# Kernel tuning notes

Measured on AMD Instinct MI355X. Metric: run time of the kernel, lower is better.

## Reference

```python
import jax, jax.numpy as jnp
import numpy as np

N, D, L = 1000, 256, 7  # nodes, feature dim, layers (hardcoded in the torch module)
B = 64


def setup_inputs() -> dict:
    key = jax.random.key(0)
    ks = jax.random.split(key, 8)
    x = jax.random.normal(ks[0], (B, N, D), dtype=jnp.float32)
    # binary adjacency mask (diagonal is forced to 1 inside reference, as in torch)
    adj = (jax.random.uniform(ks[1], (B, N, N)) < 0.05).astype(jnp.float32)
    # stacked per-layer weights; torch Linear convention: y = x @ W.T + b
    W_attn = jax.random.normal(ks[2], (L, D, D), dtype=jnp.float32) * 0.01
    b_attn = jnp.zeros((L, D), jnp.float32)
    W0 = jax.random.normal(ks[3], (L, D, D), dtype=jnp.float32) * 0.05
    b0 = jnp.zeros((L, D), jnp.float32)
    W1 = jax.random.normal(ks[4], (L, D, D), dtype=jnp.float32) * 0.05
    b1 = jnp.zeros((L, D), jnp.float32)
    Wf = jax.random.normal(ks[5], (D, D), dtype=jnp.float32) * 0.05
    bf = jnp.zeros((D,), jnp.float32)
    return {"x": x, "adj": adj, "W_attn": W_attn, "b_attn": b_attn,
            "W0": W0, "b0": b0, "W1": W1, "b1": b1, "Wf": Wf, "bf": bf}


def reference(x, adj, W_attn, b_attn, W0, b0, W1, b1, Wf, bf):
    idx = jnp.arange(N)
    adj = adj.at[:, idx, idx].set(1.0)              # self-loops forced on
    eps_eye = (1e-5 * jnp.eye(N, dtype=x.dtype))    # added before masking
    for l in range(L):
        x0 = x
        q = x @ W_attn[l].T + b_attn[l]             # [B,N,D]
        s = jax.nn.sigmoid(jnp.einsum('bid,bjd->bij', q, x))  # [B,N,N]
        s = (s + eps_eye) * adj                     # mask by adjacency
        s = s / jnp.sum(s, axis=-1, keepdims=True)  # row-sum normalize
        x = jnp.einsum('bij,bjd->bid', s, x)        # weighted aggregate
        x = jax.nn.relu(x @ W0[l].T + b0[l])
        x = jax.nn.relu(x @ W1[l].T + b1[l])
        x = x + x0                                  # residual
    return x @ Wf.T + bf
```

## Files before the change

### kernel.cpp

```cpp
#include <hip/hip_runtime.h>
#include <hip/hip_bf16.h>

#define B_ 64
#define N_ 1000
#define NP 1024
#define D_ 256
#define L_ 7
#define MP (B_*NP)
#define PKB 262144

typedef unsigned short u16;
typedef __attribute__((ext_vector_type(4))) float f32x4;
typedef __bf16 bf16x8 __attribute__((ext_vector_type(8)));

static __device__ __forceinline__ u16 f2bf(float f) {
  __hip_bfloat16 h = __float2bfloat16(f);
  return *reinterpret_cast<u16*>(&h);
}
static __device__ __forceinline__ float bf2f(u16 u) {
  __hip_bfloat16 h;
  *reinterpret_cast<u16*>(&h) = u;
  return __bfloat162float(h);
}

static __device__ __forceinline__ void gl_lds16(const u16* g, u16* l) {
  __builtin_amdgcn_global_load_lds(
      (const __attribute__((address_space(1))) void*)g,
      (__attribute__((address_space(3))) void*)l, 16, 0, 0);
}

__global__ __launch_bounds__(64) void pack_mask_k(const float* __restrict__ adj,
                                                  unsigned long long* __restrict__ mask) {
  int row = blockIdx.x;
  int b = row / N_, i = row - b * N_;
  int lane = threadIdx.x;
  const float* arow = adj + (size_t)(b * N_ + i) * N_;
  #pragma unroll
  for (int j0 = 0; j0 < NP; j0 += 64) {
    int j = j0 + lane;
    bool on = (j < N_) && (arow[j] != 0.0f || j == i);
    unsigned long long m = __ballot(on);
    if (lane == 0) mask[((size_t)(b * NP + i)) * 16 + (j0 >> 6)] = m;
  }
}

__global__ __launch_bounds__(256) void conv_w_k(const float* __restrict__ Wa,
                                                const float* __restrict__ W0,
                                                const float* __restrict__ W1,
                                                const float* __restrict__ Wf,
                                                u16* __restrict__ wpk) {
  int T = blockIdx.x * 256 + threadIdx.x;
  const int NW = 3 * L_ + 1;
  if (T >= NW * 128 * 64) return;
  int lane = T & 63;
  int fid = T >> 6;
  int k = fid & 7, f = (fid >> 3) & 3, by = (fid >> 5) & 3, w = fid >> 7;
  const float* src;
  if (w < L_) src = Wa + (size_t)w * D_ * D_;
  else if (w < 2 * L_) src = W0 + (size_t)(w - L_) * D_ * D_;
  else if (w < 3 * L_) src = W1 + (size_t)(w - 2 * L_) * D_ * D_;
  else src = Wf;
  int row = by * 64 + f * 16 + (lane & 15);
  int col = k * 32 + ((lane >> 4) << 3);
  const float* s = src + (size_t)row * D_ + col;
  u16 out8[8];
  #pragma unroll
  for (int e = 0; e < 8; e++) out8[e] = f2bf(s[e]);
  *reinterpret_cast<bf16x8*>(wpk + (size_t)T * 8) =
      *reinterpret_cast<bf16x8*>(out8);
}

__global__ __launch_bounds__(256) void prep_x_k(const float* __restrict__ x,
                                                float* __restrict__ xc,
                                                u16* __restrict__ xb) {
  size_t t = (size_t)blockIdx.x * blockDim.x + threadIdx.x;
  const size_t total = (size_t)B_ * N_ * D_;
  if (t < total) {
    int b = (int)(t / (N_ * D_));
    int rem = (int)(t - (size_t)b * (N_ * D_));
    size_t o = (size_t)b * NP * D_ + rem;
    float v = x[t];
    xc[o] = v;
    xb[o] = f2bf(v);
  }
  const size_t padTotal = (size_t)B_ * (NP - N_) * D_;
  if (t < padTotal) {
    int b = (int)(t / ((NP - N_) * D_));
    int rem = (int)(t - (size_t)b * ((NP - N_) * D_));
    size_t o = (size_t)b * NP * D_ + (size_t)N_ * D_ + rem;
    xc[o] = 0.f;
    xb[o] = 0;
  }
}

__global__ __launch_bounds__(256) void pack_both_k(const u16* __restrict__ xb,
                                                   u16* __restrict__ xpk,
                                                   u16* __restrict__ pvpk) {
  __shared__ u16 t[64][65];
  int b = blockIdx.z;
  int cc = blockIdx.x;
  int bd = blockIdx.y;
  int i0 = cc * 64, d0 = bd * 64;
  int tid = threadIdx.x;
  int tx = tid & 63, ty = tid >> 6;
  const u16* src = xb + (size_t)b * NP * D_;
  #pragma unroll
  for (int r = ty; r < 64; r += 4)
    t[r][tx] = src[(size_t)(i0 + r) * D_ + d0 + tx];
  __syncthreads();
  int lane = tid & 63, q = tid >> 6;
  int l4 = lane >> 4, l15 = lane & 15;
  int dh = bd >> 1, dcb = (bd & 1) * 4;
  u16* dstp = pvpk + (size_t)b * PKB;
  #pragma unroll
  for (int kk = 0; kk < 2; kk++) {
    int frag = cc * 32 + dh * 16 + (dcb + q) * 2 + kk;
    bf16x8 v;
    #pragma unroll
    for (int e = 0; e < 8; e++)
      v[e] = *reinterpret_cast<const __bf16*>(&t[kk * 32 + (l4 << 3) + e][q * 16 + l15]);
    *reinterpret_cast<bf16x8*>(dstp + (size_t)frag * 512 + lane * 8) = v;
  }
  u16* dstq = xpk + (size_t)b * PKB;
  #pragma unroll
  for (int kk = 0; kk < 2; kk++) {
    int frag = cc * 32 + q * 8 + (2 * bd + kk);
    bf16x8 v;
    #pragma unroll
    for (int e = 0; e < 8; e++)
      v[e] = *reinterpret_cast<const __bf16*>(&t[l15 + 16 * q][kk * 32 + (l4 << 3) + e]);
    *reinterpret_cast<bf16x8*>(dstq + (size_t)frag * 512 + lane * 8) = v;
  }
}

template <int MODE, int APK>
__global__ __launch_bounds__(256) void linear_k(const u16* __restrict__ A,
                                                const u16* __restrict__ W,
                                                const float* __restrict__ bias,
                                                u16* __restrict__ outb,
                                                float* __restrict__ xc,
                                                u16* __restrict__ xbp,
                                                float* __restrict__ outf) {
  int lane = threadIdx.x & 63;
  int wv = threadIdx.x >> 6;
  int rbase = blockIdx.x * 64 + wv * 16;
  int cbase = blockIdx.y * 64;
  f32x4 acc[4] = {};
  const u16* Ar;
  if (APK) Ar = A + ((size_t)(rbase >> 4) << 12) + lane * 8;
  else     Ar = A + (size_t)(rbase + (lane & 15)) * D_ + ((lane >> 4) << 3);
  const u16* Wr = W + (size_t)blockIdx.y * (32 * 512) + lane * 8;
  #pragma unroll
  for (int k = 0; k < 8; k++) {
    bf16x8 a = APK ? *reinterpret_cast<const bf16x8*>(Ar + k * 512)
                   : *reinterpret_cast<const bf16x8*>(Ar + k * 32);
    #pragma unroll
    for (int f = 0; f < 4; f++) {
      bf16x8 bb = *reinterpret_cast<const bf16x8*>(Wr + (f * 8 + k) * 512);
      acc[f] = __builtin_amdgcn_mfma_f32_16x16x32_bf16(a, bb, acc[f], 0, 0, 0);
    }
  }
  int r0 = rbase + ((lane >> 4) << 2);
  int col = cbase + (lane & 15);
  #pragma unroll
  for (int f = 0; f < 4; f++) {
    int c = col + f * 16;
    float bv = bias[c];
    #pragma unroll
    for (int r = 0; r < 4; r++) {
      int row = r0 + r;
      float v = acc[f][r] + bv;
      if (MODE == 3) {
        int b = row >> 10, i = row & (NP - 1);
        if (i < N_) outf[((size_t)b * N_ + i) * D_ + c] = v;
      } else {
        size_t dst = ((size_t)(row >> 4) << 12) + ((c >> 5) << 9) +
                     ((((c >> 3) & 3) * 16 + (row & 15)) << 3) + (c & 7);
        outb[dst] = f2bf(v);
      }
    }
  }
}

__global__ __launch_bounds__(256) void mlp_fused_k(const u16* __restrict__ A,
                                                   const u16* __restrict__ W0p,
                                                   const float* __restrict__ bias0,
                                                   const u16* __restrict__ W1p,
                                                   const float* __restrict__ bias1,
                                                   u16* __restrict__ xpk,
                                                   float* __restrict__ xc,
                                                   u16* __restrict__ pvpk) {
  __shared__ u16 h0lds[8192];
  int blk = blockIdx.x;
  int lane = threadIdx.x & 63;
  int wv = threadIdx.x >> 6;
  int rsub = wv & 1, ch = wv >> 1;
  int l15 = lane & 15, l4 = lane >> 4;

  const u16* Ar = A + (size_t)(blk * 32 + rsub * 16 + l15) * D_ + (l4 << 3);
  const u16* w0b = W0p + (size_t)(ch * 64) * 512 + lane * 8;
  #pragma unroll
  for (int hf = 0; hf < 2; hf++) {
    f32x4 acc1[4] = {};
    __builtin_amdgcn_s_setprio(1);
    #pragma unroll
    for (int k = 0; k < 8; k++) {
      bf16x8 a = *reinterpret_cast<const bf16x8*>(Ar + k * 32);
      #pragma unroll
      for (int ff = 0; ff < 4; ff++) {
        bf16x8 bb = *reinterpret_cast<const bf16x8*>(
            w0b + (hf * 32 + ff * 8 + k) * 512);
        acc1[ff] = __builtin_amdgcn_mfma_f32_16x16x32_bf16(a, bb, acc1[ff], 0, 0, 0);
      }
    }
    __builtin_amdgcn_s_setprio(0);
    #pragma unroll
    for (int ff = 0; ff < 4; ff++) {
      int fc = hf * 4 + ff;
      int c = ch * 128 + fc * 16 + l15;
      float bv = bias0[c];
      int base = rsub * 4096 + (ch * 4 + (fc >> 1)) * 512 +
                 (((fc * 2 + (l15 >> 3)) & 3) * 16 + l4 * 4) * 8 + (l15 & 7);
      #pragma unroll
      for (int r = 0; r < 4; r++)
        h0lds[base + r * 8] = f2bf(fmaxf(acc1[ff][r] + bv, 0.f));
    }
  }
  __syncthreads();

  const u16* w1b = W1p + (size_t)(ch * 64) * 512 + lane * 8;
  int r0g = blk * 32 + rsub * 16 + l4 * 4;
  #pragma unroll
  for (int hf = 0; hf < 2; hf++) {
    f32x4 acc2[4] = {};
    __builtin_amdgcn_s_setprio(1);
    #pragma unroll
    for (int k = 0; k < 8; k++) {
      bf16x8 a = *reinterpret_cast<const bf16x8*>(&h0lds[rsub * 4096 + k * 512 + lane * 8]);
      #pragma unroll
      for (int ff = 0; ff < 4; ff++) {
        bf16x8 bb = *reinterpret_cast<const bf16x8*>(
            w1b + (hf * 32 + ff * 8 + k) * 512);
        acc2[ff] = __builtin_amdgcn_mfma_f32_16x16x32_bf16(a, bb, acc2[ff], 0, 0, 0);
      }
    }
    __builtin_amdgcn_s_setprio(0);
    #pragma unroll
    for (int ff = 0; ff < 4; ff++) {
      int fc = hf * 4 + ff;
      int c = ch * 128 + fc * 16 + l15;
      float bv = bias1[c];
      #pragma unroll
      for (int r = 0; r < 4; r++) {
        int row = r0g + r;
        float v = fmaxf(acc2[ff][r] + bv, 0.f);
        size_t o = (size_t)row * D_ + c;
        float nv = v + xc[o];
        xc[o] = nv;
        u16 q16 = f2bf(nv);
        size_t dx = ((size_t)(row >> 4) << 12) + ((c >> 5) << 9) +
                    ((((c >> 3) & 3) * 16 + (row & 15)) << 3) + (c & 7);
        xpk[dx] = q16;
        int bb2 = row >> 10, ri = row & (NP - 1);
        size_t fragp = (size_t)(ri >> 6) * 32 + (c >> 7) * 16 +
                       (((c >> 4) & 7) * 2) + ((ri >> 5) & 1);
        size_t dp = (size_t)bb2 * PKB + fragp * 512 +
                    ((((ri >> 3) & 3) * 16 + (c & 15)) << 3) + (ri & 7);
        pvpk[dp] = q16;
      }
    }
  }
}

__global__ __launch_bounds__(512) void attn_fused_k(const u16* __restrict__ qpk,
                                                    const u16* __restrict__ xpk,
                                                    const u16* __restrict__ pvpk,
                                                    const unsigned long long* __restrict__ mask,
                                                    u16* __restrict__ yb) {
  __shared__ u16 xlds[16384];
  __shared__ u16 plds[2][64][72];
  __shared__ float dlds[8][16];
  int wg = blockIdx.x;
  int xcd = wg & 7, slot = wg >> 3;
  int b = xcd * 8 + (slot >> 4);
  int rb = slot & 15;
  int rbase = rb * 64;
  int lane = threadIdx.x & 63;
  int wv = threadIdx.x >> 6;
  int rsub = wv & 3, jh = wv >> 2;
  int l15 = lane & 15, l4 = lane >> 4;
  int rowL = rsub * 16 + l4 * 4;

  const u16* qpkB = qpk + ((((size_t)b * NP + rbase + rsub * 16) >> 4) << 12) + lane * 8;
  const u16* xpkC = xpk + (size_t)b * PKB;
  const u16* pvkB = pvpk + (size_t)b * PKB + (size_t)((wv >> 2) * 16 + (wv & 3) * 4) * 512 + lane * 8;
  const unsigned long long* mB = mask + (size_t)b * (NP * 16);

  f32x4 yacc[4][2] = {};
  float denp[4] = {0.f, 0.f, 0.f, 0.f};

  {
    const u16* gs = xpkC + wv * 2048 + lane * 8;
    u16* ld = &xlds[wv * 2048];
    #pragma unroll
    for (int i = 0; i < 4; i++)
      gl_lds16(gs + i * 512, ld + i * 512);
  }
  __syncthreads();

  #pragma unroll 1
  for (int t = 0; t < 16; t++) {
    int pb = t & 1, pr = pb ^ 1;
    f32x4 sacc[2] = {};
    __builtin_amdgcn_s_setprio(1);
    #pragma unroll
    for (int k = 0; k < 8; k++) {
      bf16x8 a = *reinterpret_cast<const bf16x8*>(qpkB + k * 512);
      bf16x8 b0 = *reinterpret_cast<const bf16x8*>(&xlds[((jh * 2) * 8 + k) * 512 + lane * 8]);
      sacc[0] = __builtin_amdgcn_mfma_f32_16x16x32_bf16(a, b0, sacc[0], 0, 0, 0);
      bf16x8 b1 = *reinterpret_cast<const bf16x8*>(&xlds[((jh * 2 + 1) * 8 + k) * 512 + lane * 8]);
      sacc[1] = __builtin_amdgcn_mfma_f32_16x16x32_bf16(a, b1, sacc[1], 0, 0, 0);
    }
    __builtin_amdgcn_s_setprio(0);
    __syncthreads();
    if (t < 15) {
      const u16* gs = xpkC + (size_t)(t + 1) * 16384 + wv * 2048 + lane * 8;
      u16* ld = &xlds[wv * 2048];
      #pragma unroll
      for (int i = 0; i < 4; i++)
        gl_lds16(gs + i * 512, ld + i * 512);
    }
    #pragma unroll
    for (int r = 0; r < 4; r++) {
      int i = rbase + rowL + r;
      unsigned long long mw = (i < N_) ? mB[((size_t)i << 4) + t] : 0ull;
      #pragma unroll
      for (int fl = 0; fl < 2; fl++) {
        int jloc = jh * 32 + fl * 16 + l15;
        int j = t * 64 + jloc;
        float w = 0.f;
        if ((mw >> jloc) & 1ull) {
          float s = 1.f / (1.f + __expf(-sacc[fl][r]));
          w = s + (i == j ? 1e-5f : 0.f);
        }
        u16 wq = f2bf(w);
        plds[pb][rowL + r][jloc] = wq;
        denp[r] += bf2f(wq);
      }
    }
    if (t > 0) {
      const u16* pvc = pvkB + (size_t)(t - 1) * (32 * 512);
      bf16x8 w00 = *reinterpret_cast<const bf16x8*>(pvc);
      bf16x8 w01 = *reinterpret_cast<const bf16x8*>(pvc + 512);
      bf16x8 w10 = *reinterpret_cast<const bf16x8*>(pvc + 1024);
      bf16x8 w11 = *reinterpret_cast<const bf16x8*>(pvc + 1536);
      __builtin_amdgcn_s_setprio(1);
      #pragma unroll
      for (int rt = 0; rt < 4; rt++) {
        bf16x8 ap0 = *reinterpret_cast<const bf16x8*>(&plds[pr][rt * 16 + l15][l4 << 3]);
        yacc[rt][0] = __builtin_amdgcn_mfma_f32_16x16x32_bf16(ap0, w00, yacc[rt][0], 0, 0, 0);
        yacc[rt][1] = __builtin_amdgcn_mfma_f32_16x16x32_bf16(ap0, w10, yacc[rt][1], 0, 0, 0);
        bf16x8 ap1 = *reinterpret_cast<const bf16x8*>(&plds[pr][rt * 16 + l15][32 + (l4 << 3)]);
        yacc[rt][0] = __builtin_amdgcn_mfma_f32_16x16x32_bf16(ap1, w01, yacc[rt][0], 0, 0, 0);
        yacc[rt][1] = __builtin_amdgcn_mfma_f32_16x16x32_bf16(ap1, w11, yacc[rt][1], 0, 0, 0);
      }
      __builtin_amdgcn_s_setprio(0);
    }
    __syncthreads();
  }

  {
    const u16* pvc = pvkB + (size_t)15 * (32 * 512);
    bf16x8 w00 = *reinterpret_cast<const bf16x8*>(pvc);
    bf16x8 w01 = *reinterpret_cast<const bf16x8*>(pvc + 512);
    bf16x8 w10 = *reinterpret_cast<const bf16x8*>(pvc + 1024);
    bf16x8 w11 = *reinterpret_cast<const bf16x8*>(pvc + 1536);
    __builtin_amdgcn_s_setprio(1);
    #pragma unroll
    for (int rt = 0; rt < 4; rt++) {
      bf16x8 ap0 = *reinterpret_cast<const bf16x8*>(&plds[1][rt * 16 + l15][l4 << 3]);
      yacc[rt][0] = __builtin_amdgcn_mfma_f32_16x16x32_bf16(ap0, w00, yacc[rt][0], 0, 0, 0);
      yacc[rt][1] = __builtin_amdgcn_mfma_f32_16x16x32_bf16(ap0, w10, yacc[rt][1], 0, 0, 0);
      bf16x8 ap1 = *reinterpret_cast<const bf16x8*>(&plds[1][rt * 16 + l15][32 + (l4 << 3)]);
      yacc[rt][0] = __builtin_amdgcn_mfma_f32_16x16x32_bf16(ap1, w01, yacc[rt][0], 0, 0, 0);
      yacc[rt][1] = __builtin_amdgcn_mfma_f32_16x16x32_bf16(ap1, w11, yacc[rt][1], 0, 0, 0);
    }
    __builtin_amdgcn_s_setprio(0);
  }

  #pragma unroll
  for (int r = 0; r < 4; r++) {
    float d = denp[r];
    #pragma unroll
    for (int m = 1; m < 16; m <<= 1) d += __shfl_xor(d, m, 64);
    if (l15 == 0) dlds[wv][l4 * 4 + r] = d;
  }
  __syncthreads();
  u16* yB = yb + ((size_t)b * NP + rbase) * D_ + wv * 32 + l15;
  #pragma unroll
  for (int rt = 0; rt < 4; rt++) {
    #pragma unroll
    for (int r = 0; r < 4; r++) {
      int rl = rt * 16 + l4 * 4 + r;
      int i = rbase + rl;
      float den = dlds[rt][l4 * 4 + r] + dlds[rt + 4][l4 * 4 + r];
      float inv = (i < N_ && den > 0.f) ? 1.f / den : 0.f;
      #pragma unroll
      for (int ct = 0; ct < 2; ct++)
        yB[(size_t)rl * D_ + ct * 16] = f2bf(yacc[rt][ct][r] * inv);
    }
  }
}

extern "C" void kernel_launch(void* const* d_in, const int* in_sizes, int n_in,
                              void* d_out, int out_size, void* d_ws, size_t ws_size,
                              hipStream_t stream) {
  const float* x   = (const float*)d_in[0];
  const float* adj = (const float*)d_in[1];
  const float* Wa  = (const float*)d_in[2];
  const float* ba  = (const float*)d_in[3];
  const float* W0  = (const float*)d_in[4];
  const float* b0_ = (const float*)d_in[5];
  const float* W1  = (const float*)d_in[6];
  const float* b1_ = (const float*)d_in[7];
  const float* Wf  = (const float*)d_in[8];
  const float* bff = (const float*)d_in[9];
  float* out = (float*)d_out;

  char* p = (char*)d_ws;
  auto alloc = [&](size_t bytes) {
    char* r = p;
    p += (bytes + 255) & ~(size_t)255;
    return r;
  };
  unsigned long long* mask = (unsigned long long*)alloc((size_t)B_ * NP * 16 * 8);
  u16* xb    = (u16*)alloc((size_t)MP * D_ * 2);
  u16* xpk   = (u16*)alloc((size_t)B_ * PKB * 2);
  u16* pvpk  = (u16*)alloc((size_t)B_ * PKB * 2);
  u16* qpk   = (u16*)alloc((size_t)MP * D_ * 2);
  u16* slotB = (u16*)alloc((size_t)MP * D_ * 2);
  float* xc  = (float*)alloc((size_t)MP * D_ * 4);
  u16* wb    = (u16*)alloc((size_t)(3 * L_ + 1) * D_ * D_ * 2);

  pack_mask_k<<<dim3(B_ * N_), dim3(64), 0, stream>>>(adj, mask);
  conv_w_k<<<dim3(704), dim3(256), 0, stream>>>(Wa, W0, W1, Wf, wb);
  prep_x_k<<<dim3((B_ * N_ * D_ + 255) / 256), dim3(256), 0, stream>>>(x, xc, xb);
  pack_both_k<<<dim3(16, 4, B_), dim3(256), 0, stream>>>(xb, xpk, pvpk);

  for (int l = 0; l < L_; l++) {
    const u16* wAttn = wb + (size_t)l * D_ * D_;
    const u16* w0l = wb + (size_t)(L_ + l) * D_ * D_;
    const u16* w1l = wb + (size_t)(2 * L_ + l) * D_ * D_;

    linear_k<4, 1><<<dim3(MP / 64, D_ / 64), dim3(256), 0, stream>>>(
        xpk, wAttn, ba + l * D_, qpk, nullptr, nullptr, nullptr);
    attn_fused_k<<<dim3(1024), dim3(512), 0, stream>>>(
        qpk, xpk, pvpk, mask, slotB);
    mlp_fused_k<<<dim3(2048), dim3(256), 0, stream>>>(
        slotB, w0l, b0_ + l * D_, w1l, b1_ + l * D_, xpk, xc, pvpk);
  }
  linear_k<3, 1><<<dim3(MP / 64, D_ / 64), dim3(256), 0, stream>>>(
      xpk, wb + (size_t)3 * L_ * D_ * D_, bff, nullptr, nullptr, nullptr, out);
}
```

Before: 1.757 ms.

## Enlarge attention row tile to 128 rows with 1024-thread workgroups

The fused attention kernel now handles 128 query rows per workgroup with 16 waves instead of 64 rows with 8 waves. Each shared X key tile loaded into LDS is reused by twice as many rows, halving global key traffic per row, and each wave now owns 16 output columns across 8 row tiles. The cost is larger LDS for the probability buffer, fewer workgroups (512), and possible occupancy or barrier overhead with 1024-thread blocks.

```diff
diff --git a/kernel.cpp b/kernel.cpp
--- a/kernel.cpp
+++ b/kernel.cpp
@@ -272,39 +272,38 @@
   }
 }
 
-__global__ __launch_bounds__(512) void attn_fused_k(const u16* __restrict__ qpk,
-                                                    const u16* __restrict__ xpk,
-                                                    const u16* __restrict__ pvpk,
-                                                    const unsigned long long* __restrict__ mask,
-                                                    u16* __restrict__ yb) {
+__global__ __launch_bounds__(1024) void attn_fused_k(const u16* __restrict__ qpk,
+                                                     const u16* __restrict__ xpk,
+                                                     const u16* __restrict__ pvpk,
+                                                     const unsigned long long* __restrict__ mask,
+                                                     u16* __restrict__ yb) {
   __shared__ u16 xlds[16384];
-  __shared__ u16 plds[2][64][72];
-  __shared__ float dlds[8][16];
+  __shared__ u16 plds[2][128][72];
+  __shared__ float dlds[16][16];
   int wg = blockIdx.x;
   int xcd = wg & 7, slot = wg >> 3;
-  int b = xcd * 8 + (slot >> 4);
-  int rb = slot & 15;
-  int rbase = rb * 64;
+  int b = xcd * 8 + (slot >> 3);
+  int rb = slot & 7;
+  int rbase = rb * 128;
   int lane = threadIdx.x & 63;
   int wv = threadIdx.x >> 6;
-  int rsub = wv & 3, jh = wv >> 2;
+  int rsub = wv >> 1, jh = wv & 1;
   int l15 = lane & 15, l4 = lane >> 4;
   int rowL = rsub * 16 + l4 * 4;
 
   const u16* qpkB = qpk + ((((size_t)b * NP + rbase + rsub * 16) >> 4) << 12) + lane * 8;
   const u16* xpkC = xpk + (size_t)b * PKB;
-  const u16* pvkB = pvpk + (size_t)b * PKB + (size_t)((wv >> 2) * 16 + (wv & 3) * 4) * 512 + lane * 8;
+  const u16* pvkB = pvpk + (size_t)b * PKB + (size_t)((wv >> 3) * 16 + (wv & 7) * 2) * 512 + lane * 8;
   const unsigned long long* mB = mask + (size_t)b * (NP * 16);
 
-  f32x4 yacc[4][2] = {};
+  f32x4 yacc[8] = {};
   float denp[4] = {0.f, 0.f, 0.f, 0.f};
 
   {
-    const u16* gs = xpkC + wv * 2048 + lane * 8;
-    u16* ld = &xlds[wv * 2048];
-    #pragma unroll
-    for (int i = 0; i < 4; i++)
-      gl_lds16(gs + i * 512, ld + i * 512);
+    const u16* gs = xpkC + wv * 1024 + lane * 8;
+    u16* ld = &xlds[wv * 1024];
+    gl_lds16(gs, ld);
+    gl_lds16(gs + 512, ld + 512);
   }
   __syncthreads();
 
@@ -324,11 +323,10 @@
     __builtin_amdgcn_s_setprio(0);
     __syncthreads();
     if (t < 15) {
-      const u16* gs = xpkC + (size_t)(t + 1) * 16384 + wv * 2048 + lane * 8;
-      u16* ld = &xlds[wv * 2048];
-      #pragma unroll
-      for (int i = 0; i < 4; i++)
-        gl_lds16(gs + i * 512, ld + i * 512);
+      const u16* gs = xpkC + (size_t)(t + 1) * 16384 + wv * 1024 + lane * 8;
+      u16* ld = &xlds[wv * 1024];
+      gl_lds16(gs, ld);
+      gl_lds16(gs + 512, ld + 512);
     }
     #pragma unroll
     for (int r = 0; r < 4; r++) {
@@ -352,17 +350,13 @@
       const u16* pvc = pvkB + (size_t)(t - 1) * (32 * 512);
       bf16x8 w00 = *reinterpret_cast<const bf16x8*>(pvc);
       bf16x8 w01 = *reinterpret_cast<const bf16x8*>(pvc + 512);
-      bf16x8 w10 = *reinterpret_cast<const bf16x8*>(pvc + 1024);
-      bf16x8 w11 = *reinterpret_cast<const bf16x8*>(pvc + 1536);
       __builtin_amdgcn_s_setprio(1);
       #pragma unroll
-      for (int rt = 0; rt < 4; rt++) {
+      for (int rt = 0; rt < 8; rt++) {
         bf16x8 ap0 = *reinterpret_cast<const bf16x8*>(&plds[pr][rt * 16 + l15][l4 << 3]);
-        yacc[rt][0] = __builtin_amdgcn_mfma_f32_16x16x32_bf16(ap0, w00, yacc[rt][0], 0, 0, 0);
-        yacc[rt][1] = __builtin_amdgcn_mfma_f32_16x16x32_bf16(ap0, w10, yacc[rt][1], 0, 0, 0);
+        yacc[rt] = __builtin_amdgcn_mfma_f32_16x16x32_bf16(ap0, w00, yacc[rt], 0, 0, 0);
         bf16x8 ap1 = *reinterpret_cast<const bf16x8*>(&plds[pr][rt * 16 + l15][32 + (l4 << 3)]);
-        yacc[rt][0] = __builtin_amdgcn_mfma_f32_16x16x32_bf16(ap1, w01, yacc[rt][0], 0, 0, 0);
-        yacc[rt][1] = __builtin_amdgcn_mfma_f32_16x16x32_bf16(ap1, w11, yacc[rt][1], 0, 0, 0);
+        yacc[rt] = __builtin_amdgcn_mfma_f32_16x16x32_bf16(ap1, w01, yacc[rt], 0, 0, 0);
       }
       __builtin_amdgcn_s_setprio(0);
     }
@@ -373,17 +367,13 @@
     const u16* pvc = pvkB + (size_t)15 * (32 * 512);
     bf16x8 w00 = *reinterpret_cast<const bf16x8*>(pvc);
     bf16x8 w01 = *reinterpret_cast<const bf16x8*>(pvc + 512);
-    bf16x8 w10 = *reinterpret_cast<const bf16x8*>(pvc + 1024);
-    bf16x8 w11 = *reinterpret_cast<const bf16x8*>(pvc + 1536);
     __builtin_amdgcn_s_setprio(1);
     #pragma unroll
-    for (int rt = 0; rt < 4; rt++) {
+    for (int rt = 0; rt < 8; rt++) {
       bf16x8 ap0 = *reinterpret_cast<const bf16x8*>(&plds[1][rt * 16 + l15][l4 << 3]);
-      yacc[rt][0] = __builtin_amdgcn_mfma_f32_16x16x32_bf16(ap0, w00, yacc[rt][0], 0, 0, 0);
-      yacc[rt][1] = __builtin_amdgcn_mfma_f32_16x16x32_bf16(ap0, w10, yacc[rt][1], 0, 0, 0);
+      yacc[rt] = __builtin_amdgcn_mfma_f32_16x16x32_bf16(ap0, w00, yacc[rt], 0, 0, 0);
       bf16x8 ap1 = *reinterpret_cast<const bf16x8*>(&plds[1][rt * 16 + l15][32 + (l4 << 3)]);
-      yacc[rt][0] = __builtin_amdgcn_mfma_f32_16x16x32_bf16(ap1, w01, yacc[rt][0], 0, 0, 0);
-      yacc[rt][1] = __builtin_amdgcn_mfma_f32_16x16x32_bf16(ap1, w11, yacc[rt][1], 0, 0, 0);
+      yacc[rt] = __builtin_amdgcn_mfma_f32_16x16x32_bf16(ap1, w01, yacc[rt], 0, 0, 0);
     }
     __builtin_amdgcn_s_setprio(0);
   }
@@ -396,18 +386,16 @@
     if (l15 == 0) dlds[wv][l4 * 4 + r] = d;
   }
   __syncthreads();
-  u16* yB = yb + ((size_t)b * NP + rbase) * D_ + wv * 32 + l15;
-  #pragma unroll
-  for (int rt = 0; rt < 4; rt++) {
+  u16* yB = yb + ((size_t)b * NP + rbase) * D_ + wv * 16 + l15;
+  #pragma unroll
+  for (int rt = 0; rt < 8; rt++) {
     #pragma unroll
     for (int r = 0; r < 4; r++) {
       int rl = rt * 16 + l4 * 4 + r;
       int i = rbase + rl;
-      float den = dlds[rt][l4 * 4 + r] + dlds[rt + 4][l4 * 4 + r];
+      float den = dlds[rt * 2][l4 * 4 + r] + dlds[rt * 2 + 1][l4 * 4 + r];
       float inv = (i < N_ && den > 0.f) ? 1.f / den : 0.f;
-      #pragma unroll
-      for (int ct = 0; ct < 2; ct++)
-        yB[(size_t)rl * D_ + ct * 16] = f2bf(yacc[rt][ct][r] * inv);
+      yB[(size_t)rl * D_] = f2bf(yacc[rt][r] * inv);
     }
   }
 }
@@ -454,7 +442,7 @@
 
     linear_k<4, 1><<<dim3(MP / 64, D_ / 64), dim3(256), 0, stream>>>(
         xpk, wAttn, ba + l * D_, qpk, nullptr, nullptr, nullptr);
-    attn_fused_k<<<dim3(1024), dim3(512), 0, stream>>>(
+    attn_fused_k<<<dim3(512), dim3(1024), 0, stream>>>(
         qpk, xpk, pvpk, mask, slotB);
     mlp_fused_k<<<dim3(2048), dim3(256), 0, stream>>>(
         slotB, w0l, b0_ + l * D_, w1l, b1_ + l * D_, xpk, xc, pvpk);
```

Result: slower. 1.824 ms (+3.8%).

## Fuse next-layer query projection and final linear into the MLP kernel

Applied to the files above, without the earlier changes.

Each MLP block now stages its new residual rows as bf16 in shared memory and immediately multiplies them by the next layer's attention weight, writing qpk directly. On the last layer the same path applies the final output projection, and the dead xc/xpk/pvpk stores are skipped. This removes a separate linear launch per layer and the re-read of xpk from global memory. In exchange it doubles the LDS footprint per block and adds a third GEMM stage to an already heavy kernel, which may reduce occupancy.

```diff
diff --git a/kernel.cpp b/kernel.cpp
--- a/kernel.cpp
+++ b/kernel.cpp
@@ -182,6 +182,7 @@
   }
 }
 
+template <int FINAL>
 __global__ __launch_bounds__(256) void mlp_fused_k(const u16* __restrict__ A,
                                                    const u16* __restrict__ W0p,
                                                    const float* __restrict__ bias0,
@@ -189,8 +190,13 @@
                                                    const float* __restrict__ bias1,
                                                    u16* __restrict__ xpk,
                                                    float* __restrict__ xc,
-                                                   u16* __restrict__ pvpk) {
+                                                   u16* __restrict__ pvpk,
+                                                   const u16* __restrict__ Wqp,
+                                                   const float* __restrict__ biasq,
+                                                   u16* __restrict__ qpk,
+                                                   float* __restrict__ outf) {
   __shared__ u16 h0lds[8192];
+  __shared__ u16 xnlds[8192];
   int blk = blockIdx.x;
   int lane = threadIdx.x & 63;
   int wv = threadIdx.x >> 6;
@@ -250,23 +256,66 @@
       int fc = hf * 4 + ff;
       int c = ch * 128 + fc * 16 + l15;
       float bv = bias1[c];
+      int base = rsub * 4096 + (ch * 4 + (fc >> 1)) * 512 +
+                 (((fc * 2 + (l15 >> 3)) & 3) * 16 + l4 * 4) * 8 + (l15 & 7);
       #pragma unroll
       for (int r = 0; r < 4; r++) {
         int row = r0g + r;
         float v = fmaxf(acc2[ff][r] + bv, 0.f);
         size_t o = (size_t)row * D_ + c;
         float nv = v + xc[o];
-        xc[o] = nv;
         u16 q16 = f2bf(nv);
-        size_t dx = ((size_t)(row >> 4) << 12) + ((c >> 5) << 9) +
-                    ((((c >> 3) & 3) * 16 + (row & 15)) << 3) + (c & 7);
-        xpk[dx] = q16;
-        int bb2 = row >> 10, ri = row & (NP - 1);
-        size_t fragp = (size_t)(ri >> 6) * 32 + (c >> 7) * 16 +
-                       (((c >> 4) & 7) * 2) + ((ri >> 5) & 1);
-        size_t dp = (size_t)bb2 * PKB + fragp * 512 +
-                    ((((ri >> 3) & 3) * 16 + (c & 15)) << 3) + (ri & 7);
-        pvpk[dp] = q16;
+        xnlds[base + r * 8] = q16;
+        if (!FINAL) {
+          xc[o] = nv;
+          size_t dx = ((size_t)(row >> 4) << 12) + ((c >> 5) << 9) +
+                      ((((c >> 3) & 3) * 16 + (row & 15)) << 3) + (c & 7);
+          xpk[dx] = q16;
+          int bb2 = row >> 10, ri = row & (NP - 1);
+          size_t fragp = (size_t)(ri >> 6) * 32 + (c >> 7) * 16 +
+                         (((c >> 4) & 7) * 2) + ((ri >> 5) & 1);
+          size_t dp = (size_t)bb2 * PKB + fragp * 512 +
+                      ((((ri >> 3) & 3) * 16 + (c & 15)) << 3) + (ri & 7);
+          pvpk[dp] = q16;
+        }
+      }
+    }
+  }
+  __syncthreads();
+
+  const u16* wqb = Wqp + (size_t)(ch * 64) * 512 + lane * 8;
+  #pragma unroll
+  for (int hf = 0; hf < 2; hf++) {
+    f32x4 acc3[4] = {};
+    __builtin_amdgcn_s_setprio(1);
+    #pragma unroll
+    for (int k = 0; k < 8; k++) {
+      bf16x8 a = *reinterpret_cast<const bf16x8*>(&xnlds[rsub * 4096 + k * 512 + lane * 8]);
+      #pragma unroll
+      for (int ff = 0; ff < 4; ff++) {
+        bf16x8 bb = *reinterpret_cast<const bf16x8*>(
+            wqb + (hf * 32 + ff * 8 + k) * 512);
+        acc3[ff] = __builtin_amdgcn_mfma_f32_16x16x32_bf16(a, bb, acc3[ff], 0, 0, 0);
+      }
+    }
+    __builtin_amdgcn_s_setprio(0);
+    #pragma unroll
+    for (int ff = 0; ff < 4; ff++) {
+      int fc = hf * 4 + ff;
+      int c = ch * 128 + fc * 16 + l15;
+      float bv = biasq[c];
+      #pragma unroll
+      for (int r = 0; r < 4; r++) {
+        int row = r0g + r;
+        float v = acc3[ff][r] + bv;
+        if (FINAL) {
+          int b = row >> 10, i = row & (NP - 1);
+          if (i < N_) outf[((size_t)b * N_ + i) * D_ + c] = v;
+        } else {
+          size_t dst = ((size_t)(row >> 4) << 12) + ((c >> 5) << 9) +
+                       ((((c >> 3) & 3) * 16 + (row & 15)) << 3) + (c & 7);
+          qpk[dst] = f2bf(v);
+        }
       }
     }
   }
@@ -447,18 +496,23 @@
   prep_x_k<<<dim3((B_ * N_ * D_ + 255) / 256), dim3(256), 0, stream>>>(x, xc, xb);
   pack_both_k<<<dim3(16, 4, B_), dim3(256), 0, stream>>>(xb, xpk, pvpk);
 
+  linear_k<4, 1><<<dim3(MP / 64, D_ / 64), dim3(256), 0, stream>>>(
+      xpk, wb, ba, qpk, nullptr, nullptr, nullptr);
+
   for (int l = 0; l < L_; l++) {
-    const u16* wAttn = wb + (size_t)l * D_ * D_;
     const u16* w0l = wb + (size_t)(L_ + l) * D_ * D_;
     const u16* w1l = wb + (size_t)(2 * L_ + l) * D_ * D_;
 
-    linear_k<4, 1><<<dim3(MP / 64, D_ / 64), dim3(256), 0, stream>>>(
-        xpk, wAttn, ba + l * D_, qpk, nullptr, nullptr, nullptr);
     attn_fused_k<<<dim3(1024), dim3(512), 0, stream>>>(
         qpk, xpk, pvpk, mask, slotB);
-    mlp_fused_k<<<dim3(2048), dim3(256), 0, stream>>>(
-        slotB, w0l, b0_ + l * D_, w1l, b1_ + l * D_, xpk, xc, pvpk);
-  }
-  linear_k<3, 1><<<dim3(MP / 64, D_ / 64), dim3(256), 0, stream>>>(
-      xpk, wb + (size_t)3 * L_ * D_ * D_, bff, nullptr, nullptr, nullptr, out);
-}
+    if (l < L_ - 1) {
+      mlp_fused_k<0><<<dim3(2048), dim3(256), 0, stream>>>(
+          slotB, w0l, b0_ + l * D_, w1l, b1_ + l * D_, xpk, xc, pvpk,
+          wb + (size_t)(l + 1) * D_ * D_, ba + (l + 1) * D_, qpk, nullptr);
+    } else {
+      mlp_fused_k<1><<<dim3(2048), dim3(256), 0, stream>>>(
+          slotB, w0l, b0_ + l * D_, w1l, b1_ + l * D_, xpk, xc, pvpk,
+          wb + (size_t)3 * L_ * D_ * D_, bff, nullptr, out);
+    }
+  }
+}
```

After: 1.727 ms. Within noise of the previous version (-1.7%).
